# Kernel tuning notes

Hardware: AMD Instinct MI355X
Metric: run time of the kernel (lower is better)

Reference implementation:

```python
import jax, jax.numpy as jnp
import numpy as np
from jax import lax

B, T = 64, 2048
D_LSTM, D_ENC, D_ATT, N_F, K = 1024, 512, 128, 32, 31
PAD = (K - 1) // 2  # 15, 'same' padding as Tacotron2 LocationLayer


def setup_inputs() -> dict:
    key = jax.random.key(0)
    ks = jax.random.split(key, 11)
    def w(k, shape, fan_in):
        return jax.random.normal(k, shape, dtype=jnp.float32) / np.sqrt(fan_in)
    return {
        "query": jax.random.normal(ks[0], (B, 1, D_LSTM), dtype=jnp.float32),
        "memory": jax.random.normal(ks[1], (B, T, D_ENC), dtype=jnp.float32),
        "attention_weights_cat": jax.random.uniform(ks[2], (B, 2, T), dtype=jnp.float32),
        "Wq": w(ks[3], (D_ATT, D_LSTM), D_LSTM),
        "bq": jnp.zeros((D_ATT,), jnp.float32),
        "Wm": w(ks[4], (D_ATT, D_ENC), D_ENC),
        "bm": jnp.zeros((D_ATT,), jnp.float32),
        "Wconv": w(ks[5], (N_F, 2, K), 2 * K),  # Conv1d weight [out, in, k], bias=False
        "Wloc": w(ks[6], (D_ATT, N_F), N_F),     # location dense, bias=False
        "Wv": w(ks[7], (1, D_ATT), D_ATT),
        "bv": jnp.zeros((1,), jnp.float32),
    }


def reference(query, memory, attention_weights_cat, Wq, bq, Wm, bm, Wconv, Wloc, Wv, bv):
    # query_layer: [B,1,D_LSTM] -> [B,1,D_ATT]
    q = query @ Wq.T + bq
    # memory_layer: [B,T,D_ENC] -> [B,T,D_ATT]
    k = memory @ Wm.T + bm
    # location_layer: Conv1d same-pad over time, then dense to D_ATT
    conv = lax.conv_general_dilated(
        attention_weights_cat, Wconv, window_strides=(1,),
        padding=[(PAD, PAD)], dimension_numbers=("NCH", "OIH", "NCH"))  # [B,N_F,T]
    loc = jnp.einsum("bft,af->bta", conv, Wloc)  # [B,T,D_ATT]
    # energies: v^T tanh(q + k + loc) -> [B,T]
    energies = (jnp.tanh(q + k + loc) @ Wv.T + bv).squeeze(-1)
    attention_weights = jax.nn.softmax(energies, axis=1)  # [B,T]
    attention_context = jnp.einsum("bt,btd->bd", attention_weights, memory)  # [B,D_ENC]
    return attention_context, attention_weights
```

## Files before the change

### kernel.cpp

```cpp
#include <hip/hip_runtime.h>
#include <math.h>

#define B_ 64
#define T_ 2048
#define DL 1024
#define DE 512
#define DA 128
#define NF 32
#define KW 31
#define PADW 15
#define TT 128
#define LDA 40

typedef short bf16x8 __attribute__((ext_vector_type(8)));
typedef float f32x4 __attribute__((ext_vector_type(4)));

__device__ __forceinline__ void split_bf16(float x, unsigned short &hi, unsigned short &lo) {
    unsigned u = __float_as_uint(x);
    unsigned short h = (unsigned short)((u + 0x7FFFu + ((u >> 16) & 1u)) >> 16);
    float hf = __uint_as_float((unsigned)h << 16);
    float l = x - hf;
    unsigned ul = __float_as_uint(l);
    hi = h;
    lo = (unsigned short)((ul + 0x7FFFu + ((ul >> 16) & 1u)) >> 16);
}

__device__ __forceinline__ float fast_tanh(float x) {
    x = fminf(fmaxf(x, -15.f), 15.f);
    float e2 = __expf(2.f * x);
    return (e2 - 1.f) * __builtin_amdgcn_rcpf(e2 + 1.f);
}

__global__ __launch_bounds__(256) void prep_kernel(const float* __restrict__ Wm,
                                                   unsigned short* __restrict__ bg_hi,
                                                   unsigned short* __restrict__ bg_lo) {
    int i = blockIdx.x * 256 + threadIdx.x;
    unsigned short h, l;
    split_bf16(Wm[i], h, l);
    bg_hi[i] = h;
    bg_lo[i] = l;
}

__global__ __launch_bounds__(128) void q_kernel(const float* __restrict__ query,
                                                const float* __restrict__ Wq,
                                                const float* __restrict__ bq,
                                                float* __restrict__ qbuf) {
    int b = blockIdx.x;
    int a = threadIdx.x;
    __shared__ __align__(16) float qs[DL];
    for (int i = threadIdx.x; i < DL; i += 128) qs[i] = query[(size_t)b * DL + i];
    __syncthreads();
    const float* wrow = Wq + (size_t)a * DL;
    float acc = 0.f;
#pragma unroll 8
    for (int i = 0; i < DL; i += 4) {
        float4 w = *(const float4*)(wrow + i);
        float4 q4 = *(const float4*)(qs + i);
        acc += w.x * q4.x + w.y * q4.y + w.z * q4.z + w.w * q4.w;
    }
    qbuf[(size_t)b * DA + a] = acc + bq[a];
}

__global__ __launch_bounds__(256, 3) void energy_kernel(
    const float* __restrict__ mem,
    const float* __restrict__ attw,
    const unsigned short* __restrict__ bg_hi,
    const unsigned short* __restrict__ bg_lo,
    const float* __restrict__ bm,
    const float* __restrict__ Wconv,
    const float* __restrict__ Wloc,
    const float* __restrict__ Wv,
    const float* __restrict__ bv,
    const float* __restrict__ qbuf,
    float* __restrict__ e_out)
{
    __shared__ __align__(16) unsigned short Ahi[TT * LDA];
    __shared__ __align__(16) unsigned short Alo[TT * LDA];
    __shared__ __align__(16) unsigned short Bhi[DA * LDA];
    __shared__ __align__(16) unsigned short Blo[DA * LDA];
    __shared__ __align__(16) float attw_s[2 * 160];
    __shared__ __align__(16) float wconv_s[NF * 64];
    __shared__ float qb_s[DA], wv_s[DA];
    __shared__ float e_part[2][TT];

    const int tid = threadIdx.x;
    const int b = blockIdx.y;
    const int t0 = blockIdx.x * TT;
    const int lane = tid & 63;
    const int wave = tid >> 6;
    const int wm = wave & 1, wn = wave >> 1;
    const int m = lane & 15;
    const int q8 = (lane >> 4) * 8;

    if (tid < DA) {
        qb_s[tid] = qbuf[(size_t)b * DA + tid] + bm[tid];
        wv_s[tid] = Wv[tid];
    }

    for (int i = tid; i < 2 * (TT + KW - 1); i += 256) {
        int c = i / 158, j = i % 158;
        int t = t0 - PADW + j;
        attw_s[c * 160 + j] = (t >= 0 && t < T_) ? attw[((size_t)b * 2 + c) * T_ + t] : 0.f;
    }
    for (int i = tid; i < NF * 2 * KW; i += 256) {
        int f = i / 62, r = i % 62;
        wconv_s[f * 64 + r] = Wconv[i];
    }
    __syncthreads();

    for (int i = tid; i < TT * NF; i += 256) {
        int t = i >> 5, f = i & 31;
        const float* w0 = wconv_s + f * 64;
        const float* a0 = attw_s + t;
        const float* a1 = attw_s + 160 + t;
        float s = 0.f;
#pragma unroll
        for (int k = 0; k < KW; ++k) s += w0[k] * a0[k] + w0[31 + k] * a1[k];
        unsigned short h, l;
        split_bf16(s, h, l);
        Ahi[t * LDA + f] = h;
        Alo[t * LDA + f] = l;
    }
    for (int i = tid; i < DA * NF; i += 256) {
        int a = i >> 5, f = i & 31;
        unsigned short h, l;
        split_bf16(Wloc[a * NF + f], h, l);
        Bhi[a * LDA + f] = h;
        Blo[a * LDA + f] = l;
    }
    __syncthreads();

    f32x4 acc[4][4];
#pragma unroll
    for (int mi = 0; mi < 4; ++mi)
#pragma unroll
        for (int ni = 0; ni < 4; ++ni) {
            f32x4 z = {0.f, 0.f, 0.f, 0.f};
            acc[mi][ni] = z;
        }

    auto mfma_step = [&]() {
        bf16x8 ah[4], al[4];
#pragma unroll
        for (int mi = 0; mi < 4; ++mi) {
            int r = (wm * 64 + mi * 16 + m) * LDA + q8;
            ah[mi] = *(const bf16x8*)(Ahi + r);
            al[mi] = *(const bf16x8*)(Alo + r);
        }
#pragma unroll
        for (int ni = 0; ni < 4; ++ni) {
            int r = (wn * 64 + ni * 16 + m) * LDA + q8;
            bf16x8 bh = *(const bf16x8*)(Bhi + r);
            bf16x8 bl = *(const bf16x8*)(Blo + r);
#pragma unroll
            for (int mi = 0; mi < 4; ++mi) {
                acc[mi][ni] = __builtin_amdgcn_mfma_f32_16x16x32_bf16(ah[mi], bh, acc[mi][ni], 0, 0, 0);
                acc[mi][ni] = __builtin_amdgcn_mfma_f32_16x16x32_bf16(ah[mi], bl, acc[mi][ni], 0, 0, 0);
                acc[mi][ni] = __builtin_amdgcn_mfma_f32_16x16x32_bf16(al[mi], bh, acc[mi][ni], 0, 0, 0);
            }
        }
    };

    mfma_step();

    const size_t mem_base = ((size_t)b * T_ + t0) * DE;
    for (int c = 0; c < 16; ++c) {
        const int k0 = c * 32;
        __syncthreads();
#pragma unroll
        for (int r = 0; r < 4; ++r) {
            int idx = tid + 256 * r;
            int t = idx >> 3, c4 = (idx & 7) * 4;
            float4 v = *(const float4*)(mem + mem_base + (size_t)t * DE + k0 + c4);
            unsigned short h0, l0, h1, l1, h2, l2, h3, l3;
            split_bf16(v.x, h0, l0);
            split_bf16(v.y, h1, l1);
            split_bf16(v.z, h2, l2);
            split_bf16(v.w, h3, l3);
            ushort4 hv = {h0, h1, h2, h3};
            ushort4 lv = {l0, l1, l2, l3};
            *(ushort4*)(Ahi + t * LDA + c4) = hv;
            *(ushort4*)(Alo + t * LDA + c4) = lv;
        }
#pragma unroll
        for (int r = 0; r < 2; ++r) {
            int idx = tid + 256 * r;
            int a = idx >> 2, c8 = (idx & 3) * 8;
            *(uint4*)(Bhi + a * LDA + c8) = *(const uint4*)(bg_hi + (size_t)a * DE + k0 + c8);
            *(uint4*)(Blo + a * LDA + c8) = *(const uint4*)(bg_lo + (size_t)a * DE + k0 + c8);
        }
        __syncthreads();
        mfma_step();
    }

    float wvr[4], qbr[4];
#pragma unroll
    for (int ni = 0; ni < 4; ++ni) {
        int a = wn * 64 + ni * 16 + m;
        wvr[ni] = wv_s[a];
        qbr[ni] = qb_s[a];
    }
    float bvv = bv[0];
#pragma unroll
    for (int mi = 0; mi < 4; ++mi) {
#pragma unroll
        for (int reg = 0; reg < 4; ++reg) {
            float s = 0.f;
#pragma unroll
            for (int ni = 0; ni < 4; ++ni)
                s += wvr[ni] * fast_tanh(acc[mi][ni][reg] + qbr[ni]);
            s += __shfl_xor(s, 1, 64);
            s += __shfl_xor(s, 2, 64);
            s += __shfl_xor(s, 4, 64);
            s += __shfl_xor(s, 8, 64);
            if (m == 0)
                e_part[wn][wm * 64 + mi * 16 + (lane >> 4) * 4 + reg] = s;
        }
    }
    __syncthreads();
    if (tid < TT)
        e_out[(size_t)b * T_ + t0 + tid] = e_part[0][tid] + e_part[1][tid] + bvv;
}

__global__ __launch_bounds__(256) void softmax_kernel(const float* __restrict__ e,
                                                      float* __restrict__ wout) {
    int b = blockIdx.x;
    int tid = threadIdx.x;
    __shared__ float red[4];
    float v[8];
    float m = -1e30f;
#pragma unroll
    for (int r = 0; r < 8; ++r) {
        v[r] = e[(size_t)b * T_ + r * 256 + tid];
        m = fmaxf(m, v[r]);
    }
#pragma unroll
    for (int off = 1; off < 64; off <<= 1) m = fmaxf(m, __shfl_xor(m, off, 64));
    if ((tid & 63) == 0) red[tid >> 6] = m;
    __syncthreads();
    m = fmaxf(fmaxf(red[0], red[1]), fmaxf(red[2], red[3]));
    __syncthreads();
    float s = 0.f;
#pragma unroll
    for (int r = 0; r < 8; ++r) {
        v[r] = expf(v[r] - m);
        s += v[r];
    }
#pragma unroll
    for (int off = 1; off < 64; off <<= 1) s += __shfl_xor(s, off, 64);
    if ((tid & 63) == 0) red[tid >> 6] = s;
    __syncthreads();
    s = red[0] + red[1] + red[2] + red[3];
    float inv = 1.0f / s;
#pragma unroll
    for (int r = 0; r < 8; ++r) wout[(size_t)b * T_ + r * 256 + tid] = v[r] * inv;
}

__global__ __launch_bounds__(256) void ctx_partial_kernel(const float* __restrict__ mem,
                                                          const float* __restrict__ w,
                                                          float* __restrict__ partial) {
    int b = blockIdx.y, tc = blockIdx.x;
    int tid = threadIdx.x;
    __shared__ float ws_s[128];
    __shared__ float red[512];
    if (tid < 128) ws_s[tid] = w[(size_t)b * T_ + tc * 128 + tid];
    __syncthreads();
    int d = (tid & 127) * 4;
    int th = tid >> 7;
    const float* mp = mem + ((size_t)b * T_ + tc * 128 + th * 64) * DE + d;
    float a0 = 0.f, a1 = 0.f, a2 = 0.f, a3 = 0.f;
#pragma unroll 8
    for (int t = 0; t < 64; ++t) {
        float4 v = *(const float4*)(mp + (size_t)t * DE);
        float wv = ws_s[th * 64 + t];
        a0 += wv * v.x; a1 += wv * v.y; a2 += wv * v.z; a3 += wv * v.w;
    }
    if (th == 1) {
        float* r = red + (tid & 127) * 4;
        r[0] = a0; r[1] = a1; r[2] = a2; r[3] = a3;
    }
    __syncthreads();
    if (th == 0) {
        const float* r = red + tid * 4;
        float* pp = partial + ((size_t)b * 16 + tc) * DE + d;
        pp[0] = a0 + r[0]; pp[1] = a1 + r[1]; pp[2] = a2 + r[2]; pp[3] = a3 + r[3];
    }
}

__global__ __launch_bounds__(512) void ctx_reduce_kernel(const float* __restrict__ partial,
                                                         float* __restrict__ ctx) {
    int b = blockIdx.x;
    int d = threadIdx.x;
    float s = 0.f;
#pragma unroll
    for (int j = 0; j < 16; ++j) s += partial[((size_t)b * 16 + j) * DE + d];
    ctx[(size_t)b * DE + d] = s;
}

extern "C" void kernel_launch(void* const* d_in, const int* in_sizes, int n_in,
                              void* d_out, int out_size, void* d_ws, size_t ws_size,
                              hipStream_t stream) {
    const float* query  = (const float*)d_in[0];
    const float* memory = (const float*)d_in[1];
    const float* attw   = (const float*)d_in[2];
    const float* Wq     = (const float*)d_in[3];
    const float* bq     = (const float*)d_in[4];
    const float* Wm     = (const float*)d_in[5];
    const float* bm     = (const float*)d_in[6];
    const float* Wconv  = (const float*)d_in[7];
    const float* Wloc   = (const float*)d_in[8];
    const float* Wv     = (const float*)d_in[9];
    const float* bv     = (const float*)d_in[10];

    float* out = (float*)d_out;
    float* ctx_out = out;
    float* w_out = out + B_ * DE;

    float* ws = (float*)d_ws;
    float* qbuf = ws;
    float* ebuf = qbuf + B_ * DA;
    float* partial = ebuf + (size_t)B_ * T_;
    unsigned short* bg_hi = (unsigned short*)(partial + (size_t)B_ * 16 * DE);
    unsigned short* bg_lo = bg_hi + DA * DE;

    prep_kernel<<<dim3(DA * DE / 256), dim3(256), 0, stream>>>(Wm, bg_hi, bg_lo);
    q_kernel<<<dim3(B_), dim3(128), 0, stream>>>(query, Wq, bq, qbuf);
    energy_kernel<<<dim3(T_ / TT, B_), dim3(256), 0, stream>>>(
        memory, attw, bg_hi, bg_lo, bm, Wconv, Wloc, Wv, bv, qbuf, ebuf);
    softmax_kernel<<<dim3(B_), dim3(256), 0, stream>>>(ebuf, w_out);
    ctx_partial_kernel<<<dim3(16, B_), dim3(256), 0, stream>>>(memory, w_out, partial);
    ctx_reduce_kernel<<<dim3(B_), dim3(512), 0, stream>>>(partial, ctx_out);
}
```

Measured before the change: 540.9 us.

## Pipeline energy GEMM with fragment-ordered LDS layout and async B loads

Reorders the A and B tiles in LDS into MFMA-fragment order, so each lane reads contiguous 16-byte fragments instead of padded row strides. The weight matrix is pre-swizzled by the prep kernel and streamed with global_load_lds into a double buffer. Memory loads for the next chunk are issued before the current MFMA step, overlapping global latency with compute. The bf16 hi/lo split of activations now truncates instead of rounding, which is cheaper but slightly changes split accuracy.

```diff
diff --git a/kernel.cpp b/kernel.cpp
--- a/kernel.cpp
+++ b/kernel.cpp
@@ -10,19 +10,27 @@
 #define KW 31
 #define PADW 15
 #define TT 128
-#define LDA 40
 
 typedef short bf16x8 __attribute__((ext_vector_type(8)));
 typedef float f32x4 __attribute__((ext_vector_type(4)));
 
-__device__ __forceinline__ void split_bf16(float x, unsigned short &hi, unsigned short &lo) {
+__device__ __forceinline__ int frag_off(int row, int kin) {
+    return (((row >> 4) * 64 + (kin >> 3) * 16 + (row & 15)) << 3) + (kin & 7);
+}
+
+__device__ __forceinline__ void split2_trunc(float x0, float x1, unsigned &h01, unsigned &l01) {
+    unsigned u0 = __float_as_uint(x0), u1 = __float_as_uint(x1);
+    h01 = __builtin_amdgcn_perm(u1, u0, 0x07060302u);
+    float l0 = x0 - __uint_as_float(u0 & 0xFFFF0000u);
+    float l1 = x1 - __uint_as_float(u1 & 0xFFFF0000u);
+    l01 = __builtin_amdgcn_perm(__float_as_uint(l1), __float_as_uint(l0), 0x07060302u);
+}
+
+__device__ __forceinline__ void split1_trunc(float x, unsigned short &h, unsigned short &l) {
     unsigned u = __float_as_uint(x);
-    unsigned short h = (unsigned short)((u + 0x7FFFu + ((u >> 16) & 1u)) >> 16);
-    float hf = __uint_as_float((unsigned)h << 16);
-    float l = x - hf;
-    unsigned ul = __float_as_uint(l);
-    hi = h;
-    lo = (unsigned short)((ul + 0x7FFFu + ((ul >> 16) & 1u)) >> 16);
+    h = (unsigned short)(u >> 16);
+    float lf = x - __uint_as_float(u & 0xFFFF0000u);
+    l = (unsigned short)(__float_as_uint(lf) >> 16);
 }
 
 __device__ __forceinline__ float fast_tanh(float x) {
@@ -32,13 +40,19 @@
 }
 
 __global__ __launch_bounds__(256) void prep_kernel(const float* __restrict__ Wm,
-                                                   unsigned short* __restrict__ bg_hi,
-                                                   unsigned short* __restrict__ bg_lo) {
+                                                   unsigned short* __restrict__ Bsw) {
     int i = blockIdx.x * 256 + threadIdx.x;
-    unsigned short h, l;
-    split_bf16(Wm[i], h, l);
-    bg_hi[i] = h;
-    bg_lo[i] = l;
+    int a = i >> 9, k = i & 511;
+    float x = Wm[i];
+    unsigned u = __float_as_uint(x);
+    unsigned short h = (unsigned short)((u + 0x7FFFu + ((u >> 16) & 1u)) >> 16);
+    float lf = x - __uint_as_float((unsigned)h << 16);
+    unsigned ul = __float_as_uint(lf);
+    unsigned short l = (unsigned short)((ul + 0x7FFFu + ((ul >> 16) & 1u)) >> 16);
+    int c = k >> 5, kin = k & 31;
+    size_t base = (size_t)c * 8192 + frag_off(a, kin);
+    Bsw[base] = h;
+    Bsw[base + 4096] = l;
 }
 
 __global__ __launch_bounds__(128) void q_kernel(const float* __restrict__ query,
@@ -64,8 +78,7 @@
 __global__ __launch_bounds__(256, 3) void energy_kernel(
     const float* __restrict__ mem,
     const float* __restrict__ attw,
-    const unsigned short* __restrict__ bg_hi,
-    const unsigned short* __restrict__ bg_lo,
+    const unsigned short* __restrict__ Bsw,
     const float* __restrict__ bm,
     const float* __restrict__ Wconv,
     const float* __restrict__ Wloc,
@@ -74,12 +87,8 @@
     const float* __restrict__ qbuf,
     float* __restrict__ e_out)
 {
-    __shared__ __align__(16) unsigned short Ahi[TT * LDA];
-    __shared__ __align__(16) unsigned short Alo[TT * LDA];
-    __shared__ __align__(16) unsigned short Bhi[DA * LDA];
-    __shared__ __align__(16) unsigned short Blo[DA * LDA];
-    __shared__ __align__(16) float attw_s[2 * 160];
-    __shared__ __align__(16) float wconv_s[NF * 64];
+    __shared__ __align__(16) unsigned short Abuf[8192];
+    __shared__ __align__(16) unsigned short Bbuf[2][8192];
     __shared__ float qb_s[DA], wv_s[DA];
     __shared__ float e_part[2][TT];
 
@@ -90,7 +99,9 @@
     const int wave = tid >> 6;
     const int wm = wave & 1, wn = wave >> 1;
     const int m = lane & 15;
-    const int q8 = (lane >> 4) * 8;
+
+    float* attw_s  = (float*)Bbuf[1];
+    float* wconv_s = (float*)Bbuf[1] + 320;
 
     if (tid < DA) {
         qb_s[tid] = qbuf[(size_t)b * DA + tid] + bm[tid];
@@ -105,6 +116,14 @@
     for (int i = tid; i < NF * 2 * KW; i += 256) {
         int f = i / 62, r = i % 62;
         wconv_s[f * 64 + r] = Wconv[i];
+    }
+    for (int i = tid; i < DA * NF; i += 256) {
+        int a = i >> 5, f = i & 31;
+        unsigned short h, l;
+        split1_trunc(Wloc[a * NF + f], h, l);
+        int off = frag_off(a, f);
+        Bbuf[0][off] = h;
+        Bbuf[0][off + 4096] = l;
     }
     __syncthreads();
 
@@ -117,16 +136,10 @@
 #pragma unroll
         for (int k = 0; k < KW; ++k) s += w0[k] * a0[k] + w0[31 + k] * a1[k];
         unsigned short h, l;
-        split_bf16(s, h, l);
-        Ahi[t * LDA + f] = h;
-        Alo[t * LDA + f] = l;
-    }
-    for (int i = tid; i < DA * NF; i += 256) {
-        int a = i >> 5, f = i & 31;
-        unsigned short h, l;
-        split_bf16(Wloc[a * NF + f], h, l);
-        Bhi[a * LDA + f] = h;
-        Blo[a * LDA + f] = l;
+        split1_trunc(s, h, l);
+        int off = frag_off(t, f);
+        Abuf[off] = h;
+        Abuf[off + 4096] = l;
     }
     __syncthreads();
 
@@ -139,19 +152,19 @@
             acc[mi][ni] = z;
         }
 
-    auto mfma_step = [&]() {
+    auto mfma_step = [&](const unsigned short* Bb) {
         bf16x8 ah[4], al[4];
 #pragma unroll
         for (int mi = 0; mi < 4; ++mi) {
-            int r = (wm * 64 + mi * 16 + m) * LDA + q8;
-            ah[mi] = *(const bf16x8*)(Ahi + r);
-            al[mi] = *(const bf16x8*)(Alo + r);
+            const unsigned short* p = Abuf + (((wm * 4 + mi) * 64 + lane) << 3);
+            ah[mi] = *(const bf16x8*)p;
+            al[mi] = *(const bf16x8*)(p + 4096);
         }
 #pragma unroll
         for (int ni = 0; ni < 4; ++ni) {
-            int r = (wn * 64 + ni * 16 + m) * LDA + q8;
-            bf16x8 bh = *(const bf16x8*)(Bhi + r);
-            bf16x8 bl = *(const bf16x8*)(Blo + r);
+            const unsigned short* p = Bb + (((wn * 4 + ni) * 64 + lane) << 3);
+            bf16x8 bh = *(const bf16x8*)p;
+            bf16x8 bl = *(const bf16x8*)(p + 4096);
 #pragma unroll
             for (int mi = 0; mi < 4; ++mi) {
                 acc[mi][ni] = __builtin_amdgcn_mfma_f32_16x16x32_bf16(ah[mi], bh, acc[mi][ni], 0, 0, 0);
@@ -161,36 +174,56 @@
         }
     };
 
-    mfma_step();
+    auto issue_B = [&](int c, unsigned short* dst) {
+        const unsigned char* g = (const unsigned char*)Bsw + (size_t)c * 16384 + wave * 4096 + lane * 16;
+        unsigned char* l = (unsigned char*)dst + wave * 4096;
+#pragma unroll
+        for (int it = 0; it < 4; ++it)
+            __builtin_amdgcn_global_load_lds(
+                (const __attribute__((address_space(1))) unsigned*)(g + it * 1024),
+                (__attribute__((address_space(3))) unsigned*)(l + it * 1024), 16, 0, 0);
+    };
 
     const size_t mem_base = ((size_t)b * T_ + t0) * DE;
+    const int tA = tid >> 3;
+    const int c4 = (tid & 7) * 4;
+
+    float4 ap[4];
+    auto load_A = [&](int c) {
+        const float* p = mem + mem_base + (size_t)tA * DE + c * 32 + c4;
+#pragma unroll
+        for (int r = 0; r < 4; ++r) ap[r] = *(const float4*)(p + (size_t)r * 32 * DE);
+    };
+    auto store_A = [&]() {
+        int off0 = frag_off(tA, c4);
+#pragma unroll
+        for (int r = 0; r < 4; ++r) {
+            unsigned h01, l01, h23, l23;
+            split2_trunc(ap[r].x, ap[r].y, h01, l01);
+            split2_trunc(ap[r].z, ap[r].w, h23, l23);
+            int off = off0 + r * 1024;
+            uint2 hv = {h01, h23}, lv = {l01, l23};
+            *(uint2*)(Abuf + off) = hv;
+            *(uint2*)(Abuf + off + 4096) = lv;
+        }
+    };
+
+    mfma_step(Bbuf[0]);
+    load_A(0);
+    __syncthreads();
+    issue_B(0, Bbuf[0]);
+    store_A();
+    __syncthreads();
+
     for (int c = 0; c < 16; ++c) {
-        const int k0 = c * 32;
+        if (c < 15) {
+            load_A(c + 1);
+            issue_B(c + 1, Bbuf[(c + 1) & 1]);
+        }
+        mfma_step(Bbuf[c & 1]);
         __syncthreads();
-#pragma unroll
-        for (int r = 0; r < 4; ++r) {
-            int idx = tid + 256 * r;
-            int t = idx >> 3, c4 = (idx & 7) * 4;
-            float4 v = *(const float4*)(mem + mem_base + (size_t)t * DE + k0 + c4);
-            unsigned short h0, l0, h1, l1, h2, l2, h3, l3;
-            split_bf16(v.x, h0, l0);
-            split_bf16(v.y, h1, l1);
-            split_bf16(v.z, h2, l2);
-            split_bf16(v.w, h3, l3);
-            ushort4 hv = {h0, h1, h2, h3};
-            ushort4 lv = {l0, l1, l2, l3};
-            *(ushort4*)(Ahi + t * LDA + c4) = hv;
-            *(ushort4*)(Alo + t * LDA + c4) = lv;
-        }
-#pragma unroll
-        for (int r = 0; r < 2; ++r) {
-            int idx = tid + 256 * r;
-            int a = idx >> 2, c8 = (idx & 3) * 8;
-            *(uint4*)(Bhi + a * LDA + c8) = *(const uint4*)(bg_hi + (size_t)a * DE + k0 + c8);
-            *(uint4*)(Blo + a * LDA + c8) = *(const uint4*)(bg_lo + (size_t)a * DE + k0 + c8);
-        }
+        if (c < 15) store_A();
         __syncthreads();
-        mfma_step();
     }
 
     float wvr[4], qbr[4];
@@ -320,13 +353,12 @@
     float* qbuf = ws;
     float* ebuf = qbuf + B_ * DA;
     float* partial = ebuf + (size_t)B_ * T_;
-    unsigned short* bg_hi = (unsigned short*)(partial + (size_t)B_ * 16 * DE);
-    unsigned short* bg_lo = bg_hi + DA * DE;
-
-    prep_kernel<<<dim3(DA * DE / 256), dim3(256), 0, stream>>>(Wm, bg_hi, bg_lo);
+    unsigned short* Bsw = (unsigned short*)(partial + (size_t)B_ * 16 * DE);
+
+    prep_kernel<<<dim3(DA * DE / 256), dim3(256), 0, stream>>>(Wm, Bsw);
     q_kernel<<<dim3(B_), dim3(128), 0, stream>>>(query, Wq, bq, qbuf);
     energy_kernel<<<dim3(T_ / TT, B_), dim3(256), 0, stream>>>(
-        memory, attw, bg_hi, bg_lo, bm, Wconv, Wloc, Wv, bv, qbuf, ebuf);
+        memory, attw, Bsw, bm, Wconv, Wloc, Wv, bv, qbuf, ebuf);
     softmax_kernel<<<dim3(B_), dim3(256), 0, stream>>>(ebuf, w_out);
     ctx_partial_kernel<<<dim3(16, B_), dim3(256), 0, stream>>>(memory, w_out, partial);
     ctx_reduce_kernel<<<dim3(B_), dim3(512), 0, stream>>>(partial, ctx_out);
```

Measured after the change: 567.9 us. 5.0% more time.
